# Kernel tuning notes

Hardware: AMD Instinct MI355X
Metric: run time of the kernel (lower is better)

The kernel has to match this reference:

```python
import jax, jax.numpy as jnp
import numpy as np

H = 16  # num_heads (d_model=1024, d_head=64)


def setup_inputs() -> dict:
    key = jax.random.key(0)
    ks = jax.random.split(key, 10)
    B, L, S, G, D = 8, 1024, 1024, 64, 1024
    s = 0.02  # keep score magnitudes sane for softmax
    return {
        "queries": jax.random.normal(ks[0], (B, L, D), jnp.float32),
        "keys": jax.random.normal(ks[1], (B, S, D), jnp.float32),
        "values": jax.random.normal(ks[2], (B, S, D), jnp.float32),
        "routers": jax.random.normal(ks[3], (B, G, D), jnp.float32),
        "Wq": jax.random.normal(ks[4], (D, D), jnp.float32) * s,
        "Wk": jax.random.normal(ks[5], (D, D), jnp.float32) * s,
        "Wv": jax.random.normal(ks[6], (D, D), jnp.float32) * s,
        "Wlq": jax.random.normal(ks[7], (D, D), jnp.float32) * s,
        "Wlk": jax.random.normal(ks[8], (D, D), jnp.float32) * s,
        "Wo": jax.random.normal(ks[9], (D, D), jnp.float32) * s,
        "bo": jnp.zeros((D,), jnp.float32),
    }


def reference(queries, keys, values, routers, Wq, Wk, Wv, Wlq, Wlk, Wo, bo):
    B, L, _ = queries.shape
    S = keys.shape[1]
    d_head = queries.shape[-1] // H
    scale = d_head ** (-0.5)

    def split_heads(x, W, n):
        # (B,n,d_model) @ (d_model,H*d_head) -> (B,H,n,d_head)
        return (x @ W).reshape(B, n, H, d_head).transpose(0, 2, 1, 3)

    q = split_heads(queries, Wq, L)
    k = split_heads(keys, Wk, S)
    v = split_heads(values, Wv, S)
    rq = split_heads(routers, Wlq, routers.shape[1])
    rk = split_heads(routers, Wlk, routers.shape[1])

    # learned per-head bilinear electrode-position matrix: (B,H,d,d)
    W_ep = jnp.einsum('bhgd,bhge->bhde', rq, rk)
    # bilinear QK scores: q . W_ep . k^T
    scores = jnp.einsum('bhld,bhde,bhke->bhlk', q, W_ep, k) * scale
    attn = jax.nn.softmax(scores, axis=-1)  # (B,H,L,S)
    out = jnp.einsum('bhlk,bhkd->bhld', attn, v)  # (B,H,L,d_head)
    # faithful to original: transpose(-2,-1) then view(B,L,-1)
    out = jnp.swapaxes(out, -2, -1).reshape(B, L, H * d_head)
    return out @ Wo + bo
```

## Files before the change

### kernel.cpp

```cpp
#include <hip/hip_runtime.h>

typedef __bf16 bf16;
typedef short s8v __attribute__((ext_vector_type(8)));
typedef float f4v __attribute__((ext_vector_type(4)));
typedef bf16 bf4v __attribute__((ext_vector_type(4)));
typedef bf16 bf8v __attribute__((ext_vector_type(8)));

#define NH 16
#define BB 8
#define QWSCALE 0.18033688011112043f

__device__ __forceinline__ void glds16(void* lds, const void* g) {
    __builtin_amdgcn_global_load_lds(
        (const __attribute__((address_space(1))) unsigned int*)g,
        (__attribute__((address_space(3))) unsigned int*)lds, 16, 0, 0);
}

__global__ __launch_bounds__(256) void rgemm_k(
    const float* __restrict__ A, const float* __restrict__ W1, const float* __restrict__ W2,
    float* __restrict__ C1, float* __restrict__ C2)
{
    __shared__ float As[16][68];
    __shared__ float Bs[16][36];
    const int tid = threadIdx.x;
    const int bm = blockIdx.x;
    int bn = blockIdx.y;
    const float* W = (bn < 32) ? W1 : W2;
    float* C = (bn < 32) ? C1 : C2;
    if (bn >= 32) bn -= 32;
    const int h = bn >> 1;
    const int dq = (bn & 1) * 32;
    const int n0 = h * 64 + dq;

    const int ar = tid >> 2, ac = (tid & 3) * 4;
    const int br = tid >> 3, bc = (tid & 7) * 4;
    const int tr = (tid >> 4) * 4, tc = (tid & 15) * 2;

    float acc[4][2];
#pragma unroll
    for (int i = 0; i < 4; i++) { acc[i][0] = 0.f; acc[i][1] = 0.f; }

    for (int kt = 0; kt < 1024; kt += 16) {
        float4 av = *(const float4*)&A[(size_t)(bm * 64 + ar) * 1024 + kt + ac];
        float4 bv;
        if (tid < 128) bv = *(const float4*)&W[(size_t)(kt + br) * 1024 + n0 + bc];
        __syncthreads();
        As[ac + 0][ar] = av.x; As[ac + 1][ar] = av.y;
        As[ac + 2][ar] = av.z; As[ac + 3][ar] = av.w;
        if (tid < 128) *(float4*)&Bs[br][bc] = bv;
        __syncthreads();
#pragma unroll
        for (int k = 0; k < 16; k++) {
            float4 x = *(const float4*)&As[k][tr];
            float2 y = *(const float2*)&Bs[k][tc];
            float xv[4] = {x.x, x.y, x.z, x.w};
#pragma unroll
            for (int i = 0; i < 4; i++) {
                acc[i][0] += xv[i] * y.x;
                acc[i][1] += xv[i] * y.y;
            }
        }
    }

#pragma unroll
    for (int i = 0; i < 4; i++) {
        float2 v = make_float2(acc[i][0], acc[i][1]);
        *(float2*)&C[((size_t)(bm * NH + h) * 64 + tr + i) * 64 + dq + tc] = v;
    }
}

__global__ __launch_bounds__(256) void wep_k(
    const float* __restrict__ RQ, const float* __restrict__ RK, float* __restrict__ WEP)
{
    const int bh = blockIdx.x;
    __shared__ float rqs[4096];
    __shared__ float rks[4096];
    const int tid = threadIdx.x;
    const float4* rq4 = (const float4*)(RQ + (size_t)bh * 4096);
    const float4* rk4 = (const float4*)(RK + (size_t)bh * 4096);
#pragma unroll
    for (int j = 0; j < 4; j++) {
        ((float4*)rqs)[tid + 256 * j] = rq4[tid + 256 * j];
        ((float4*)rks)[tid + 256 * j] = rk4[tid + 256 * j];
    }
    __syncthreads();
    const int dd = tid >> 2, q = (tid & 3) * 16;
    float acc[16];
#pragma unroll
    for (int i = 0; i < 16; i++) acc[i] = 0.f;
    for (int g = 0; g < 64; g++) {
        float a = rqs[g * 64 + dd];
#pragma unroll
        for (int i = 0; i < 16; i++) acc[i] += a * rks[g * 64 + q + i];
    }
    float* out = WEP + (size_t)bh * 4096 + dd * 64 + q;
#pragma unroll
    for (int i4 = 0; i4 < 4; i4++)
        *(float4*)&out[i4 * 4] =
            make_float4(acc[i4 * 4], acc[i4 * 4 + 1], acc[i4 * 4 + 2], acc[i4 * 4 + 3]);
}

__global__ __launch_bounds__(256) void wqwep_k(
    const float* __restrict__ Wq, const float* __restrict__ WEP,
    bf16* __restrict__ Thi, bf16* __restrict__ Tlo)
{
    const int bh = blockIdx.x;
    const int b = bh >> 4, h = bh & 15;
    const int Dt = blockIdx.y;
    __shared__ float weps[4096];
    __shared__ float wqs[128 * 68];
    const int tid = threadIdx.x;
    const float4* wsrc = (const float4*)(WEP + (size_t)bh * 4096);
#pragma unroll
    for (int it = 0; it < 4; it++)
        ((float4*)weps)[it * 256 + tid] = wsrc[it * 256 + tid];
#pragma unroll
    for (int it = 0; it < 8; it++) {
        int g = it * 256 + tid;
        int r = g >> 4, c = (g & 15) * 4;
        *(float4*)&wqs[r * 68 + c] =
            *(const float4*)&Wq[(size_t)(Dt * 128 + r) * 1024 + h * 64 + c];
    }
    __syncthreads();
    const int Dloc = tid >> 1, e0 = (tid & 1) * 32;
    float acc[32];
#pragma unroll
    for (int e = 0; e < 32; e++) acc[e] = 0.f;
    for (int d = 0; d < 64; d++) {
        float a = wqs[Dloc * 68 + d];
        const float* wr = &weps[d * 64 + e0];
#pragma unroll
        for (int e = 0; e < 32; e++) acc[e] += a * wr[e];
    }
    __syncthreads();
    unsigned* stage = (unsigned*)wqs;
#pragma unroll
    for (int e = 0; e < 32; e++) {
        float v = acc[e] * QWSCALE;
        bf16 hv = (bf16)v;
        bf16 lv = (bf16)(v - (float)hv);
        unsigned hb = *(unsigned short*)&hv;
        unsigned lb = *(unsigned short*)&lv;
        stage[(e0 + e) * 132 + Dloc] = hb | (lb << 16);
    }
    __syncthreads();
    {
        const int e = tid >> 2, c0 = (tid & 3) * 32;
        const unsigned* src = &stage[e * 132 + c0];
        bf16 hi32[32], lo32[32];
#pragma unroll
        for (int j = 0; j < 32; j++) {
            unsigned u = src[j];
            unsigned short hb = (unsigned short)(u & 0xffff);
            unsigned short lb = (unsigned short)(u >> 16);
            hi32[j] = *(bf16*)&hb;
            lo32[j] = *(bf16*)&lb;
        }
        size_t base = ((size_t)b * 1024 + h * 64 + e) * 1024 + Dt * 128 + c0;
#pragma unroll
        for (int q8 = 0; q8 < 4; q8++) {
            *(bf8v*)&Thi[base + q8 * 8] = *(bf8v*)&hi32[q8 * 8];
            *(bf8v*)&Tlo[base + q8 * 8] = *(bf8v*)&lo32[q8 * 8];
        }
    }
}

__global__ void split_cast_k(const float* __restrict__ x, bf16* __restrict__ hi,
                             bf16* __restrict__ lo, int n4)
{
    int idx = blockIdx.x * blockDim.x + threadIdx.x;
    int stride = gridDim.x * blockDim.x;
    for (int i = idx; i < n4; i += stride) {
        float4 v = ((const float4*)x)[i];
        bf4v h;
        h[0] = (bf16)v.x; h[1] = (bf16)v.y; h[2] = (bf16)v.z; h[3] = (bf16)v.w;
        ((bf4v*)hi)[i] = h;
        if (lo) {
            bf4v l;
            l[0] = (bf16)(v.x - (float)h[0]);
            l[1] = (bf16)(v.y - (float)h[1]);
            l[2] = (bf16)(v.z - (float)h[2]);
            l[3] = (bf16)(v.w - (float)h[3]);
            ((bf4v*)lo)[i] = l;
        }
    }
}

__global__ __launch_bounds__(256) void transw_k(const float* __restrict__ W,
                                                bf16* __restrict__ WT, bf16* __restrict__ WTlo)
{
    __shared__ float T[64 * 68];
    const int k0 = blockIdx.x * 64, n0 = blockIdx.y * 64;
    const int tid = threadIdx.x;
#pragma unroll
    for (int it = 0; it < 4; it++) {
        int g = it * 256 + tid;
        int r = g >> 4, c = (g & 15) * 4;
        *(float4*)&T[r * 68 + c] = *(const float4*)&W[(size_t)(k0 + r) * 1024 + n0 + c];
    }
    __syncthreads();
#pragma unroll
    for (int it = 0; it < 4; it++) {
        int g = it * 256 + tid;
        int n = g >> 4, k4 = (g & 15) * 4;
        bf4v o, ol;
#pragma unroll
        for (int t = 0; t < 4; t++) {
            float v = T[(k4 + t) * 68 + n];
            o[t] = (bf16)v;
            ol[t] = (bf16)(v - (float)o[t]);
        }
        *(bf4v*)&WT[(size_t)(n0 + n) * 1024 + k0 + k4] = o;
        if (WTlo) *(bf4v*)&WTlo[(size_t)(n0 + n) * 1024 + k0 + k4] = ol;
    }
}

template<int PASSES>
__global__ __launch_bounds__(256, 2) void gemm_k(
    const bf16* __restrict__ A, const bf16* __restrict__ Alo,
    const bf16* __restrict__ Bt, const bf16* __restrict__ Btlo,
    int bBatched, int outmode,
    float* __restrict__ outF, const float* __restrict__ bias,
    bf16* __restrict__ outH, bf16* __restrict__ outL)
{
    __shared__ bf16 Ah[128 * 64];
    __shared__ bf16 Bh[128 * 64];
    __shared__ bf16 Al[(PASSES == 3) ? 128 * 64 : 64];
    __shared__ bf16 Bl[(PASSES == 3) ? 128 * 64 : 64];
    const int tid = threadIdx.x;
    const int bm = blockIdx.x, bn = blockIdx.y;
    const size_t boff = bBatched ? ((size_t)(bm >> 3) << 20) : (size_t)0;
    const bf16* Bt_b = Bt + boff;
    const bf16* Btlo_b = (PASSES == 3) ? (Btlo + boff) : nullptr;
    const int li = tid & 15;
    const int qq = (tid >> 4) & 3;
    const int wave = tid >> 6;
    const int wm0 = (wave & 1) * 64, wn0 = (wave >> 1) * 64;

    f4v acc[4][4];
    f4v zf; zf[0] = 0.f; zf[1] = 0.f; zf[2] = 0.f; zf[3] = 0.f;
#pragma unroll
    for (int mt = 0; mt < 4; mt++)
#pragma unroll
        for (int nt = 0; nt < 4; nt++) acc[mt][nt] = zf;

    for (int kt = 0; kt < 16; kt++) {
        const int col0 = kt * 64;
#pragma unroll
        for (int it = 0; it < 4; it++) {
            int g = it * 256 + tid;
            int r = g >> 3, p = g & 7;
            int gcol = col0 + ((p ^ (r & 7)) << 3);
            int ldsoff = (g & ~63) << 3;
            size_t ga = (size_t)(bm * 128 + r) * 1024 + gcol;
            size_t gb = (size_t)(bn * 128 + r) * 1024 + gcol;
            glds16(Ah + ldsoff, A + ga);
            glds16(Bh + ldsoff, Bt_b + gb);
            if (PASSES == 3) {
                glds16(Al + ldsoff, Alo + ga);
                glds16(Bl + ldsoff, Btlo_b + gb);
            }
        }
        __syncthreads();
#pragma unroll
        for (int ks = 0; ks < 2; ks++) {
            s8v af[4], alf[4], bhf[4], blf[4];
#pragma unroll
            for (int mt = 0; mt < 4; mt++) {
                int row = wm0 + mt * 16 + li;
                int off = row * 64 + (((ks * 4 + qq) ^ (li & 7)) << 3);
                af[mt] = *(const s8v*)&Ah[off];
                if (PASSES == 3) alf[mt] = *(const s8v*)&Al[off];
            }
#pragma unroll
            for (int nt = 0; nt < 4; nt++) {
                int row = wn0 + nt * 16 + li;
                int off = row * 64 + (((ks * 4 + qq) ^ (li & 7)) << 3);
                bhf[nt] = *(const s8v*)&Bh[off];
                if (PASSES == 3) blf[nt] = *(const s8v*)&Bl[off];
            }
#pragma unroll
            for (int mt = 0; mt < 4; mt++)
#pragma unroll
                for (int nt = 0; nt < 4; nt++) {
                    acc[mt][nt] = __builtin_amdgcn_mfma_f32_16x16x32_bf16(
                        af[mt], bhf[nt], acc[mt][nt], 0, 0, 0);
                    if (PASSES == 3) {
                        acc[mt][nt] = __builtin_amdgcn_mfma_f32_16x16x32_bf16(
                            alf[mt], bhf[nt], acc[mt][nt], 0, 0, 0);
                        acc[mt][nt] = __builtin_amdgcn_mfma_f32_16x16x32_bf16(
                            af[mt], blf[nt], acc[mt][nt], 0, 0, 0);
                    }
                }
        }
        __syncthreads();
    }

#pragma unroll
    for (int mt = 0; mt < 4; mt++) {
#pragma unroll
        for (int nt = 0; nt < 4; nt++) {
            int n = bn * 128 + wn0 + nt * 16 + li;
            int m0 = bm * 128 + wm0 + mt * 16 + qq * 4;
            if (outmode == 0) {
                float bv = bias[n];
#pragma unroll
                for (int rg = 0; rg < 4; rg++)
                    outF[(size_t)(m0 + rg) * 1024 + n] = acc[mt][nt][rg] + bv;
            } else if (outmode == 1) {
                int h = n >> 6, e = n & 63;
#pragma unroll
                for (int rg = 0; rg < 4; rg++) {
                    int m = m0 + rg;
                    int b = m >> 10, l = m & 1023;
                    size_t idx = ((size_t)(b * NH + h) * 1024 + l) * 64 + e;
                    float v = acc[mt][nt][rg];
                    bf16 hv = (bf16)v;
                    outH[idx] = hv;
                    outL[idx] = (bf16)(v - (float)hv);
                }
            } else {
                int b = m0 >> 10, s = m0 & 1023;
                int h = n >> 6, d = n & 63;
                bf4v v;
                v[0] = (bf16)acc[mt][nt][0]; v[1] = (bf16)acc[mt][nt][1];
                v[2] = (bf16)acc[mt][nt][2]; v[3] = (bf16)acc[mt][nt][3];
                *(bf4v*)&outH[((size_t)(b * NH + h) * 64 + d) * 1024 + s] = v;
            }
        }
    }
}

__global__ __launch_bounds__(256, 2) void attn_k(
    const bf16* __restrict__ QwHi, const bf16* __restrict__ QwLo,
    const bf16* __restrict__ KpHi, const bf16* __restrict__ KpLo,
    const bf16* __restrict__ VT, bf16* __restrict__ O)
{
    __shared__ __align__(16) char scratch[43008];
    bf16* Kh = (bf16*)scratch;
    bf16* Kl = Kh + 4096;
    bf16* Vt = Kh + 8192;
    bf16* Pb = Kh + 12288;
    float* Obuf = (float*)scratch;

    const int tid = threadIdx.x;
    const int w = blockIdx.x;
    const int idx = w >> 3;
    const int l0 = (idx & 7) * 128;
    const int bh = (w & 7) + 8 * (idx >> 3);
    const int li = tid & 15;
    const int qq = (tid >> 4) & 3;
    const int wave = tid >> 6;
    const int r0w = wave * 32;

    s8v qhf[2][2], qlf[2][2];
    {
        const bf16* qh = QwHi + ((size_t)bh * 1024 + l0) * 64;
        const bf16* ql = QwLo + ((size_t)bh * 1024 + l0) * 64;
#pragma unroll
        for (int rt = 0; rt < 2; rt++) {
            int row = r0w + rt * 16 + li;
#pragma unroll
            for (int ks = 0; ks < 2; ks++) {
                int off = row * 64 + (ks * 4 + qq) * 8;
                qhf[rt][ks] = *(const s8v*)&qh[off];
                qlf[rt][ks] = *(const s8v*)&ql[off];
            }
        }
    }

    float mrun[2], lsum[2];
    mrun[0] = -__builtin_inff(); mrun[1] = -__builtin_inff();
    lsum[0] = 0.f; lsum[1] = 0.f;
    f4v accO[4][2];
    {
        f4v zf; zf[0] = 0.f; zf[1] = 0.f; zf[2] = 0.f; zf[3] = 0.f;
#pragma unroll
        for (int dt = 0; dt < 4; dt++) { accO[dt][0] = zf; accO[dt][1] = zf; }
    }

    for (int s0 = 0; s0 < 1024; s0 += 64) {
        __syncthreads();
#pragma unroll
        for (int it = 0; it < 6; it++) {
            int g = it * 256 + tid;
            int buf = g >> 9;
            int L = g & 511;
            int r = L >> 3, p = L & 7;
            int blk = (p ^ (r & 7)) << 3;
            const bf16* src;
            bf16* dstb;
            if (buf == 0)      { src = KpHi + ((size_t)bh * 1024 + s0 + r) * 64 + blk; dstb = Kh; }
            else if (buf == 1) { src = KpLo + ((size_t)bh * 1024 + s0 + r) * 64 + blk; dstb = Kl; }
            else               { src = VT + ((size_t)bh * 64 + r) * 1024 + s0 + blk;   dstb = Vt; }
            glds16(dstb + ((L & ~63) << 3), src);
        }
        __syncthreads();

        f4v accS[4][2];
        {
            f4v zf; zf[0] = 0.f; zf[1] = 0.f; zf[2] = 0.f; zf[3] = 0.f;
#pragma unroll
            for (int ct = 0; ct < 4; ct++) { accS[ct][0] = zf; accS[ct][1] = zf; }
        }
#pragma unroll
        for (int ks = 0; ks < 2; ks++) {
            s8v khf[4], klf[4];
#pragma unroll
            for (int ct = 0; ct < 4; ct++) {
                int row = ct * 16 + li;
                int off = row * 64 + (((ks * 4 + qq) ^ (li & 7)) << 3);
                khf[ct] = *(const s8v*)&Kh[off];
                klf[ct] = *(const s8v*)&Kl[off];
            }
#pragma unroll
            for (int ct = 0; ct < 4; ct++)
#pragma unroll
                for (int rt = 0; rt < 2; rt++) {
                    accS[ct][rt] = __builtin_amdgcn_mfma_f32_16x16x32_bf16(
                        khf[ct], qhf[rt][ks], accS[ct][rt], 0, 0, 0);
                    accS[ct][rt] = __builtin_amdgcn_mfma_f32_16x16x32_bf16(
                        khf[ct], qlf[rt][ks], accS[ct][rt], 0, 0, 0);
                    accS[ct][rt] = __builtin_amdgcn_mfma_f32_16x16x32_bf16(
                        klf[ct], qhf[rt][ks], accS[ct][rt], 0, 0, 0);
                }
        }

#pragma unroll
        for (int rt = 0; rt < 2; rt++) {
            float mx = -1e30f;
#pragma unroll
            for (int ct = 0; ct < 4; ct++)
#pragma unroll
                for (int rg = 0; rg < 4; rg++) mx = fmaxf(mx, accS[ct][rt][rg]);
            mx = fmaxf(mx, __shfl_xor(mx, 16));
            mx = fmaxf(mx, __shfl_xor(mx, 32));
            if (!__all(mx - mrun[rt] <= 8.f)) {
                float mnew = fmaxf(mrun[rt], mx);
                float alpha = exp2f(mrun[rt] - mnew);
                lsum[rt] *= alpha;
                mrun[rt] = mnew;
#pragma unroll
                for (int dt = 0; dt < 4; dt++)
#pragma unroll
                    for (int rg = 0; rg < 4; rg++) accO[dt][rt][rg] *= alpha;
            }
            float ls = 0.f;
            int prow = r0w + rt * 16 + li;
#pragma unroll
            for (int ct = 0; ct < 4; ct++) {
                bf4v pv;
#pragma unroll
                for (int rg = 0; rg < 4; rg++) {
                    float p_ = exp2f(accS[ct][rt][rg] - mrun[rt]);
                    ls += p_;
                    pv[rg] = (bf16)p_;
                }
                *(bf4v*)&Pb[prow * 72 + ct * 16 + qq * 4] = pv;
            }
            ls += __shfl_xor(ls, 16);
            ls += __shfl_xor(ls, 32);
            lsum[rt] += ls;
        }
        asm volatile("" ::: "memory");

#pragma unroll
        for (int ks = 0; ks < 2; ks++) {
            s8v vf[4], pf[2];
#pragma unroll
            for (int dt = 0; dt < 4; dt++) {
                int row = dt * 16 + li;
                int off = row * 64 + (((ks * 4 + qq) ^ (li & 7)) << 3);
                vf[dt] = *(const s8v*)&Vt[off];
            }
#pragma unroll
            for (int rt = 0; rt < 2; rt++) {
                int row = r0w + rt * 16 + li;
                pf[rt] = *(const s8v*)&Pb[row * 72 + ks * 32 + qq * 8];
            }
#pragma unroll
            for (int dt = 0; dt < 4; dt++)
#pragma unroll
                for (int rt = 0; rt < 2; rt++)
                    accO[dt][rt] = __builtin_amdgcn_mfma_f32_16x16x32_bf16(
                        vf[dt], pf[rt], accO[dt][rt], 0, 0, 0);
        }
    }

    __syncthreads();
#pragma unroll
    for (int rt = 0; rt < 2; rt++) {
        float inv = 1.f / lsum[rt];
        int rr = r0w + rt * 16 + li;
#pragma unroll
        for (int dt = 0; dt < 4; dt++)
#pragma unroll
            for (int rg = 0; rg < 4; rg++)
                Obuf[(dt * 16 + qq * 4 + rg) * 132 + rr] = accO[dt][rt][rg] * inv;
    }
    __syncthreads();
    {
        int d = tid >> 2, c0 = (tid & 3) * 32;
        const float* src = &Obuf[d * 132 + c0];
        bf16* dst = O + ((size_t)bh * 64 + d) * 1024 + l0 + c0;
#pragma unroll
        for (int q8 = 0; q8 < 4; q8++) {
            bf8v o;
#pragma unroll
            for (int j = 0; j < 8; j++) o[j] = (bf16)src[q8 * 8 + j];
            *(bf8v*)&dst[q8 * 8] = o;
        }
    }
}

extern "C" void kernel_launch(void* const* d_in, const int* in_sizes, int n_in,
                              void* d_out, int out_size, void* d_ws, size_t ws_size,
                              hipStream_t stream) {
    const float* queries = (const float*)d_in[0];
    const float* keys    = (const float*)d_in[1];
    const float* values  = (const float*)d_in[2];
    const float* routers = (const float*)d_in[3];
    const float* Wq  = (const float*)d_in[4];
    const float* Wk  = (const float*)d_in[5];
    const float* Wv  = (const float*)d_in[6];
    const float* Wlq = (const float*)d_in[7];
    const float* Wlk = (const float*)d_in[8];
    const float* Wo  = (const float*)d_in[9];
    const float* bo  = (const float*)d_in[10];
    float* out = (float*)d_out;

    char* w = (char*)d_ws;
    const size_t BIG = 16777216;
    bf16* QwHi = (bf16*)(w);
    bf16* QwLo = (bf16*)(w + 1 * BIG);
    bf16* Thi  = (bf16*)(w + 2 * BIG);
    bf16* Tlo  = (bf16*)(w + 3 * BIG);
    bf16* actHi = (bf16*)(w + 4 * BIG);
    bf16* actLo = (bf16*)(w + 5 * BIG);
    char* w2 = w + 6 * BIG;
    const size_t SM = 2097152;
    bf16*  WkThi = (bf16*)(w2);
    bf16*  WkTlo = (bf16*)(w2 + 1 * SM);
    bf16*  WvT   = (bf16*)(w2 + 2 * SM);
    bf16*  WoT   = (bf16*)(w2 + 3 * SM);
    float* RQ    = (float*)(w2 + 4 * SM);
    float* RK    = (float*)(w2 + 5 * SM);
    float* WEP   = (float*)(w2 + 6 * SM);
    bf16* KpHi = Thi;
    bf16* KpLo = Tlo;
    bf16* VTp  = actLo;
    bf16* Obf  = actHi;

    dim3 blk(256);
    transw_k<<<dim3(16, 16), blk, 0, stream>>>(Wk, WkThi, WkTlo);
    transw_k<<<dim3(16, 16), blk, 0, stream>>>(Wv, WvT, nullptr);
    transw_k<<<dim3(16, 16), blk, 0, stream>>>(Wo, WoT, nullptr);
    rgemm_k<<<dim3(8, 64), blk, 0, stream>>>(routers, Wlq, Wlk, RQ, RK);
    wep_k<<<dim3(BB * NH), blk, 0, stream>>>(RQ, RK, WEP);
    wqwep_k<<<dim3(BB * NH, 8), blk, 0, stream>>>(Wq, WEP, Thi, Tlo);
    split_cast_k<<<1024, blk, 0, stream>>>(queries, actHi, actLo, 2097152);
    gemm_k<3><<<dim3(64, 8), blk, 0, stream>>>(actHi, actLo, Thi, Tlo, 1, 1,
                                               nullptr, nullptr, QwHi, QwLo);
    split_cast_k<<<1024, blk, 0, stream>>>(keys, actHi, actLo, 2097152);
    gemm_k<3><<<dim3(64, 8), blk, 0, stream>>>(actHi, actLo, WkThi, WkTlo, 0, 1,
                                               nullptr, nullptr, KpHi, KpLo);
    split_cast_k<<<1024, blk, 0, stream>>>(values, actHi, nullptr, 2097152);
    gemm_k<1><<<dim3(64, 8), blk, 0, stream>>>(actHi, nullptr, WvT, nullptr, 0, 2,
                                               nullptr, nullptr, VTp, nullptr);
    attn_k<<<dim3(1024), blk, 0, stream>>>(QwHi, QwLo, KpHi, KpLo, VTp, Obf);
    gemm_k<1><<<dim3(64, 8), blk, 0, stream>>>(Obf, nullptr, WoT, nullptr, 0, 0,
                                               out, bo, nullptr, nullptr);
}
```

Measured before the change: 540.1 us.

## Stage split-head GEMM epilogue through LDS and merge weight transposes

In outmode 1, the GEMM epilogue now packs hi/lo bf16 results into shared memory, then writes contiguous 16-byte vectors per row into the head-split layout. The old version issued scattered 2-byte stores. The three weight-transpose launches are also merged into one launch indexed by blockIdx.z. The epilogue adds two barriers per half and reuses the A/B tile LDS as staging space. The shared-memory declaration moves to a single aliased char buffer.

```diff
diff --git a/kernel.cpp b/kernel.cpp
--- a/kernel.cpp
+++ b/kernel.cpp
@@ -186,9 +186,15 @@
     }
 }
 
-__global__ __launch_bounds__(256) void transw_k(const float* __restrict__ W,
-                                                bf16* __restrict__ WT, bf16* __restrict__ WTlo)
+__global__ __launch_bounds__(256) void transw3_k(
+    const float* __restrict__ W0, const float* __restrict__ W1, const float* __restrict__ W2,
+    bf16* __restrict__ T0, bf16* __restrict__ T0lo, bf16* __restrict__ T1, bf16* __restrict__ T2)
 {
+    const float* W;
+    bf16 *WT, *WTlo;
+    if (blockIdx.z == 0)      { W = W0; WT = T0; WTlo = T0lo; }
+    else if (blockIdx.z == 1) { W = W1; WT = T1; WTlo = nullptr; }
+    else                      { W = W2; WT = T2; WTlo = nullptr; }
     __shared__ float T[64 * 68];
     const int k0 = blockIdx.x * 64, n0 = blockIdx.y * 64;
     const int tid = threadIdx.x;
@@ -223,10 +229,12 @@
     float* __restrict__ outF, const float* __restrict__ bias,
     bf16* __restrict__ outH, bf16* __restrict__ outL)
 {
-    __shared__ bf16 Ah[128 * 64];
-    __shared__ bf16 Bh[128 * 64];
-    __shared__ bf16 Al[(PASSES == 3) ? 128 * 64 : 64];
-    __shared__ bf16 Bl[(PASSES == 3) ? 128 * 64 : 64];
+    __shared__ __align__(16) char smem[(PASSES == 3) ? 65536 : 34048];
+    bf16* Ah = (bf16*)smem;
+    bf16* Bh = Ah + 8192;
+    bf16* Al = Bh + 8192;
+    bf16* Bl = Al + ((PASSES == 3) ? 8192 : 64);
+    unsigned* stage = (unsigned*)smem;
     const int tid = threadIdx.x;
     const int bm = blockIdx.x, bn = blockIdx.y;
     const size_t boff = bBatched ? ((size_t)(bm >> 3) << 20) : (size_t)0;
@@ -296,36 +304,71 @@
         __syncthreads();
     }
 
-#pragma unroll
-    for (int mt = 0; mt < 4; mt++) {
-#pragma unroll
-        for (int nt = 0; nt < 4; nt++) {
-            int n = bn * 128 + wn0 + nt * 16 + li;
-            int m0 = bm * 128 + wm0 + mt * 16 + qq * 4;
-            if (outmode == 0) {
-                float bv = bias[n];
-#pragma unroll
-                for (int rg = 0; rg < 4; rg++)
-                    outF[(size_t)(m0 + rg) * 1024 + n] = acc[mt][nt][rg] + bv;
-            } else if (outmode == 1) {
-                int h = n >> 6, e = n & 63;
-#pragma unroll
-                for (int rg = 0; rg < 4; rg++) {
-                    int m = m0 + rg;
-                    int b = m >> 10, l = m & 1023;
-                    size_t idx = ((size_t)(b * NH + h) * 1024 + l) * 64 + e;
-                    float v = acc[mt][nt][rg];
-                    bf16 hv = (bf16)v;
-                    outH[idx] = hv;
-                    outL[idx] = (bf16)(v - (float)hv);
+    if (outmode == 1) {
+#pragma unroll
+        for (int p = 0; p < 2; p++) {
+            __syncthreads();
+            if ((wave & 1) == p) {
+#pragma unroll
+                for (int mt = 0; mt < 4; mt++)
+#pragma unroll
+                    for (int nt = 0; nt < 4; nt++)
+#pragma unroll
+                        for (int rg = 0; rg < 4; rg++) {
+                            float v = acc[mt][nt][rg];
+                            bf16 hv = (bf16)v;
+                            bf16 lv = (bf16)(v - (float)hv);
+                            unsigned hb = *(unsigned short*)&hv;
+                            unsigned lb = *(unsigned short*)&lv;
+                            stage[(mt * 16 + qq * 4 + rg) * 132 + wn0 + nt * 16 + li] =
+                                hb | (lb << 16);
+                        }
+            }
+            __syncthreads();
+            {
+                int mloc = tid >> 2, quarter = tid & 3;
+                int hh = quarter >> 1, e0 = (quarter & 1) * 32;
+                int m = bm * 128 + 64 * p + mloc;
+                int b = m >> 10, l = m & 1023;
+                int h = bn * 2 + hh;
+                const unsigned* src = &stage[mloc * 132 + hh * 64 + e0];
+                bf16 hi32[32], lo32[32];
+#pragma unroll
+                for (int j = 0; j < 32; j++) {
+                    unsigned u = src[j];
+                    unsigned short hb = (unsigned short)(u & 0xffff);
+                    unsigned short lb = (unsigned short)(u >> 16);
+                    hi32[j] = *(bf16*)&hb;
+                    lo32[j] = *(bf16*)&lb;
                 }
-            } else {
-                int b = m0 >> 10, s = m0 & 1023;
-                int h = n >> 6, d = n & 63;
-                bf4v v;
-                v[0] = (bf16)acc[mt][nt][0]; v[1] = (bf16)acc[mt][nt][1];
-                v[2] = (bf16)acc[mt][nt][2]; v[3] = (bf16)acc[mt][nt][3];
-                *(bf4v*)&outH[((size_t)(b * NH + h) * 64 + d) * 1024 + s] = v;
+                size_t base = ((size_t)(b * NH + h) * 1024 + l) * 64 + e0;
+#pragma unroll
+                for (int q8 = 0; q8 < 4; q8++) {
+                    *(bf8v*)&outH[base + q8 * 8] = *(bf8v*)&hi32[q8 * 8];
+                    *(bf8v*)&outL[base + q8 * 8] = *(bf8v*)&lo32[q8 * 8];
+                }
+            }
+        }
+    } else {
+#pragma unroll
+        for (int mt = 0; mt < 4; mt++) {
+#pragma unroll
+            for (int nt = 0; nt < 4; nt++) {
+                int n = bn * 128 + wn0 + nt * 16 + li;
+                int m0 = bm * 128 + wm0 + mt * 16 + qq * 4;
+                if (outmode == 0) {
+                    float bv = bias ? bias[n] : 0.f;
+#pragma unroll
+                    for (int rg = 0; rg < 4; rg++)
+                        outF[(size_t)(m0 + rg) * 1024 + n] = acc[mt][nt][rg] + bv;
+                } else {
+                    int b = m0 >> 10, s = m0 & 1023;
+                    int h = n >> 6, d = n & 63;
+                    bf4v v;
+                    v[0] = (bf16)acc[mt][nt][0]; v[1] = (bf16)acc[mt][nt][1];
+                    v[2] = (bf16)acc[mt][nt][2]; v[3] = (bf16)acc[mt][nt][3];
+                    *(bf4v*)&outH[((size_t)(b * NH + h) * 64 + d) * 1024 + s] = v;
+                }
             }
         }
     }
@@ -552,9 +595,7 @@
     bf16* Obf  = actHi;
 
     dim3 blk(256);
-    transw_k<<<dim3(16, 16), blk, 0, stream>>>(Wk, WkThi, WkTlo);
-    transw_k<<<dim3(16, 16), blk, 0, stream>>>(Wv, WvT, nullptr);
-    transw_k<<<dim3(16, 16), blk, 0, stream>>>(Wo, WoT, nullptr);
+    transw3_k<<<dim3(16, 16, 3), blk, 0, stream>>>(Wk, Wv, Wo, WkThi, WkTlo, WvT, WoT);
     rgemm_k<<<dim3(8, 64), blk, 0, stream>>>(routers, Wlq, Wlk, RQ, RK);
     wep_k<<<dim3(BB * NH), blk, 0, stream>>>(RQ, RK, WEP);
     wqwep_k<<<dim3(BB * NH, 8), blk, 0, stream>>>(Wq, WEP, Thi, Tlo);
```

New measurement: 531.3 us. Within noise of the previous version (-1.6%).
